# Optimization experiments

Hardware: AMD Instinct MI355X
Metric: run time of the kernel (lower is better)

The kernel has to match this reference:

```python
import jax, jax.numpy as jnp
import numpy as np

B, H, W, C = 1, 180, 360, 192
WS, SHIFT, NH = 6, 3, 6
MLAT, MLON = H // WS, W // WS
NW = MLAT * MLON
N = WS * WS
HD = C // NH
SCALE = HD ** -0.5
EPS = 1e-5


def _rel_index():
    # earth-specific relative position index: (MLAT, N, N) int32
    ch = np.arange(WS)
    cw = np.arange(WS)
    coords = np.stack(np.meshgrid(ch, cw, indexing='ij')).reshape(2, -1)  # (2, N)
    rel = coords[:, :, None] - coords[:, None, :]                         # (2, N, N)
    idx = (rel[0] + WS - 1) * (2 * WS - 1) + (rel[1] + WS - 1)            # (N, N)
    off = np.arange(MLAT) * (2 * WS - 1) * (2 * WS - 1)                   # per-latitude offset
    return (idx[None, :, :] + off[:, None, None]).astype(np.int32)


def _attn_mask():
    # standard shifted-window mask: (NW, N, N), 0 or -100
    img = np.zeros((H, W), dtype=np.int32)
    cnt = 0
    for hs in (slice(0, -WS), slice(-WS, -SHIFT), slice(-SHIFT, None)):
        for ws_ in (slice(0, -WS), slice(-WS, -SHIFT), slice(-SHIFT, None)):
            img[hs, ws_] = cnt
            cnt += 1
    wins = img.reshape(MLAT, WS, MLON, WS).transpose(0, 2, 1, 3).reshape(NW, N)
    diff = wins[:, None, :] - wins[:, :, None]
    return np.where(diff != 0, -100.0, 0.0).astype(np.float32)

_RPI = jnp.asarray(_rel_index())     # (MLAT, N, N)
_MASK = jnp.asarray(_attn_mask())    # (NW, N, N)


def _layernorm(x, g, b):
    mu = jnp.mean(x, axis=-1, keepdims=True)
    var = jnp.mean(jnp.square(x - mu), axis=-1, keepdims=True)
    return (x - mu) * jax.lax.rsqrt(var + EPS) * g + b


def _window_partition(x):
    # (B, H, W, C) -> (B*NW, N, C)
    x = x.reshape(B, MLAT, WS, MLON, WS, C).transpose(0, 1, 3, 2, 4, 5)
    return x.reshape(B * NW, N, C)


def _window_reverse(w):
    # (B*NW, N, C) -> (B, H, W, C)
    x = w.reshape(B, MLAT, MLON, WS, WS, C).transpose(0, 1, 3, 2, 4, 5)
    return x.reshape(B, H, W, C)


def setup_inputs() -> dict:
    key = jax.random.key(0)
    ks = jax.random.split(key, 6)
    s = 0.02
    return {
        'x': jax.random.normal(ks[0], (B, H * W, C), jnp.float32),
        'norm1_w': jnp.ones((C,), jnp.float32),
        'norm1_b': jnp.zeros((C,), jnp.float32),
        'qkv_w': jax.random.normal(ks[1], (C, 3 * C), jnp.float32) * s,
        'qkv_b': jnp.zeros((3 * C,), jnp.float32),
        'proj_w': jax.random.normal(ks[2], (C, C), jnp.float32) * s,
        'proj_b': jnp.zeros((C,), jnp.float32),
        'bias_table': jax.random.normal(ks[3], (MLAT * (2 * WS - 1) ** 2, NH), jnp.float32) * s,
        'norm2_w': jnp.ones((C,), jnp.float32),
        'norm2_b': jnp.zeros((C,), jnp.float32),
        'fc1_w': jax.random.normal(ks[4], (C, 4 * C), jnp.float32) * s,
        'fc1_b': jnp.zeros((4 * C,), jnp.float32),
        'fc2_w': jax.random.normal(ks[5], (4 * C, C), jnp.float32) * s,
        'fc2_b': jnp.zeros((C,), jnp.float32),
    }


def reference(x, norm1_w, norm1_b, qkv_w, qkv_b, proj_w, proj_b, bias_table,
              norm2_w, norm2_b, fc1_w, fc1_b, fc2_w, fc2_b):
    shortcut = x
    h = _layernorm(x, norm1_w, norm1_b).reshape(B, H, W, C)
    # cyclic shift
    h = jnp.roll(h, shift=(-SHIFT, -SHIFT), axis=(1, 2))
    xw = _window_partition(h)                                   # (B*NW, N, C)

    qkv = xw @ qkv_w + qkv_b                                    # (B_, N, 3C)
    qkv = qkv.reshape(B * NW, N, 3, NH, HD).transpose(2, 0, 3, 1, 4)
    q, k, v = qkv[0], qkv[1], qkv[2]                            # (B_, NH, N, HD)

    # earth-specific relative position bias, gathered per latitude row
    bias = jnp.take(bias_table, _RPI, axis=0)                   # (MLAT, N, N, NH)
    bias = bias.transpose(0, 3, 1, 2)[:, None]                  # (MLAT, 1, NH, N, N)
    bias = jnp.broadcast_to(bias, (MLAT, MLON, NH, N, N)).reshape(NW, NH, N, N)
    bias = bias + _MASK[:, None]                                # add shift mask

    attn = jnp.einsum('bhnd,bhmd->bhnm', q, k) * SCALE + bias
    attn = jax.nn.softmax(attn, axis=-1)
    av = jnp.einsum('bhnm,bhmd->bhnd', attn, v)                 # (B_, NH, N, HD)
    av = av.transpose(0, 2, 1, 3).reshape(B * NW, N, C)
    av = av @ proj_w + proj_b

    h = _window_reverse(av)
    h = jnp.roll(h, shift=(SHIFT, SHIFT), axis=(1, 2)).reshape(B, H * W, C)
    x = shortcut + h

    m = _layernorm(x, norm2_w, norm2_b)
    m = jax.nn.gelu(m @ fc1_w + fc1_b, approximate=False) @ fc2_w + fc2_b
    return x + m
```

## Files before the change

### kernel.cpp

```cpp
#include <hip/hip_runtime.h>
#include <hip/hip_bf16.h>

constexpr int HH   = 180;
constexpr int WW   = 360;
constexpr int CC   = 192;
constexpr int WS   = 6;
constexpr int SHIFT= 3;
constexpr int NH   = 6;
constexpr int MLAT = HH / WS;
constexpr int MLON = WW / WS;
constexpr int NWIN = MLAT * MLON;
constexpr int NTOK = WS * WS;
constexpr int HD   = CC / NH;
constexpr long M_TOK = (long)NWIN * NTOK;
constexpr long M_PAD = 65024;
constexpr float SCALE_F = 0.17677669529663687f;

typedef unsigned short ushort_t;
using bf16x8 = __attribute__((ext_vector_type(8))) short;
using f32x4  = __attribute__((ext_vector_type(4))) float;

static __device__ inline float b2f(ushort_t u) {
    union { float f; unsigned int i; } v; v.i = ((unsigned int)u) << 16; return v.f;
}
static __device__ inline ushort_t f2b(float f) {
    __hip_bfloat16 h = __float2bfloat16(f);
    return *(ushort_t*)&h;
}
static __device__ inline unsigned int cvtpk(float lo, float hi) {
    unsigned int r;
    asm("v_cvt_pk_bf16_f32 %0, %1, %2" : "=v"(r) : "v"(lo), "v"(hi));
    return r;
}

static __device__ inline void gload_lds16(const ushort_t* g, ushort_t* l) {
    __builtin_amdgcn_global_load_lds(
        (const __attribute__((address_space(1))) unsigned int*)g,
        (__attribute__((address_space(3))) unsigned int*)l, 16, 0, 0);
}

__global__ void transpose_f2b(const float* __restrict__ in, ushort_t* __restrict__ out,
                              int K, int N) {
    int e = blockIdx.x * 256 + threadIdx.x;
    if (e >= K * N) return;
    int n = e / K, k = e - n * K;
    out[e] = f2b(in[(long)k * N + n]);
}

__global__ void zero_bf16(ushort_t* __restrict__ p, int count) {
    int e = blockIdx.x * 256 + threadIdx.x;
    if (e < count) p[e] = 0;
}

static __device__ inline int region1d(int p, int L) {
    return (p < L - WS) ? 0 : ((p < L - SHIFT) ? 1 : 2);
}

__global__ void bias_mask_precompute(const float* __restrict__ bt, float* __restrict__ bm) {
    int idx = blockIdx.x * 256 + threadIdx.x;
    if (idx >= MLAT * 2 * NH * 36 * 48) return;
    int e = idx;
    int j = e % 48; e /= 48;
    int i = e % 36; e /= 36;
    int h = e % NH; e /= NH;
    int lt = e % 2;
    int mlat = e / 2;
    if (j >= 36) { bm[idx] = -1e30f; return; }
    int ih = i / WS, iw = i - ih * WS;
    int jh = j / WS, jw = j - jh * WS;
    int bidx = mlat * 121 + (ih - jh + 5) * 11 + (iw - jw + 5);
    float v = bt[bidx * NH + h];
    int mlon = lt ? (MLON - 1) : 0;
    int ri = region1d(mlat * WS + ih, HH) * 3 + region1d(mlon * WS + iw, WW);
    int rj = region1d(mlat * WS + jh, HH) * 3 + region1d(mlon * WS + jw, WW);
    if (ri != rj) v += -100.0f;
    bm[idx] = v;
}

__global__ __launch_bounds__(256) void ln1_window_kernel(
    const float* __restrict__ x, const float* __restrict__ g, const float* __restrict__ b,
    ushort_t* __restrict__ xw)
{
    long t = (long)blockIdx.x * 4 + (threadIdx.x >> 6);
    int lane = threadIdx.x & 63;
    if (t >= M_PAD) return;
    if (t >= M_TOK) {
        ushort_t* o = xw + t * CC;
        o[lane] = 0; o[lane + 64] = 0; o[lane + 128] = 0;
        return;
    }
    int ti = (int)t;
    int w = ti / NTOK, n = ti - w * NTOK;
    int mlat = w / MLON, mlon = w - mlat * MLON;
    int sh = mlat * WS + n / WS, sw = mlon * WS + (n % WS);
    int hh = sh + SHIFT; if (hh >= HH) hh -= HH;
    int ww = sw + SHIFT; if (ww >= WW) ww -= WW;
    const float* row = x + ((long)hh * WW + ww) * CC;
    float v0 = row[lane], v1 = row[lane + 64], v2 = row[lane + 128];
    float s = v0 + v1 + v2;
    float ss = v0 * v0 + v1 * v1 + v2 * v2;
    #pragma unroll
    for (int o = 32; o > 0; o >>= 1) { s += __shfl_xor(s, o, 64); ss += __shfl_xor(ss, o, 64); }
    float mu = s * (1.0f / CC);
    float var = ss * (1.0f / CC) - mu * mu;
    float rinv = rsqrtf(var + 1e-5f);
    ushort_t* o = xw + t * CC;
    o[lane]       = f2b((v0 - mu) * rinv * g[lane]       + b[lane]);
    o[lane + 64]  = f2b((v1 - mu) * rinv * g[lane + 64]  + b[lane + 64]);
    o[lane + 128] = f2b((v2 - mu) * rinv * g[lane + 128] + b[lane + 128]);
}

__global__ __launch_bounds__(256) void ln2_kernel(
    const float* __restrict__ xin, const float* __restrict__ g, const float* __restrict__ b,
    ushort_t* __restrict__ h2)
{
    long t = (long)blockIdx.x * 4 + (threadIdx.x >> 6);
    int lane = threadIdx.x & 63;
    if (t >= M_PAD) return;
    if (t >= M_TOK) {
        ushort_t* o = h2 + t * CC;
        o[lane] = 0; o[lane + 64] = 0; o[lane + 128] = 0;
        return;
    }
    const float* row = xin + t * CC;
    float v0 = row[lane], v1 = row[lane + 64], v2 = row[lane + 128];
    float s = v0 + v1 + v2;
    float ss = v0 * v0 + v1 * v1 + v2 * v2;
    #pragma unroll
    for (int o = 32; o > 0; o >>= 1) { s += __shfl_xor(s, o, 64); ss += __shfl_xor(ss, o, 64); }
    float mu = s * (1.0f / CC);
    float var = ss * (1.0f / CC) - mu * mu;
    float rinv = rsqrtf(var + 1e-5f);
    ushort_t* o = h2 + t * CC;
    o[lane]       = f2b((v0 - mu) * rinv * g[lane]       + b[lane]);
    o[lane + 64]  = f2b((v1 - mu) * rinv * g[lane + 64]  + b[lane + 64]);
    o[lane + 128] = f2b((v2 - mu) * rinv * g[lane + 128] + b[lane + 128]);
}

#define BM 128
#define BN 192
#define BK 32

template<int MODE, int KK>
__global__ __launch_bounds__(512, 3) void gemm_bf16(
    const ushort_t* __restrict__ A, const ushort_t* __restrict__ Bt,
    const float* __restrict__ bias,
    ushort_t* __restrict__ outb, float* __restrict__ outf,
    const float* __restrict__ resid,
    int N, long Mguard, int ncol, int nwg)
{
    constexpr int nk = KK / BK;
    __shared__ __align__(16) ushort_t lds[20480];
    __shared__ int row_map[BM];

    int tid = threadIdx.x;
    int lane = tid & 63;
    int wid = tid >> 6;
    int lr = lane & 15, lg = lane >> 4;
    int wm = wid >> 2, wn = wid & 3;

    int orig = blockIdx.x;
    int q = nwg >> 3, r8 = nwg & 7;
    int xcd = orig & 7, pos = orig >> 3;
    int wg = (xcd < r8 ? xcd * (q + 1) : r8 * (q + 1) + (xcd - r8) * q) + pos;
    int brow = wg / ncol, bcol = wg - brow * ncol;
    long bm0 = (long)brow * BM;
    int n0 = bcol * BN;

    if (MODE == 2 && tid < BM) {
        long t = bm0 + tid;
        if (t < M_TOK) {
            int ti = (int)t;
            int w = ti / NTOK, n = ti - w * NTOK;
            int mlat = w / MLON, mlon = w - mlat * MLON;
            int sh = mlat * WS + n / WS, sw = mlon * WS + (n % WS);
            int hh = sh + SHIFT; if (hh >= HH) hh -= HH;
            int wv = sw + SHIFT; if (wv >= WW) wv -= WW;
            row_map[tid] = hh * WW + wv;
        } else row_map[tid] = -1;
    }

    int a_pos  = tid * 16;
    int a_row  = a_pos >> 6, a_cb = a_pos & 63;
    int a_scol = (a_cb ^ ((a_row & 3) << 4)) >> 1;
    int b_row  = a_row, b_scol = a_scol;
    int b2_pos = 8192 + a_pos;
    int b2_row = b2_pos >> 6, b2_cb = b2_pos & 63;
    int b2_scol = (b2_cb ^ ((b2_row & 3) << 4)) >> 1;

#define STAGE(b, k0) do { \
    char* base = (char*)lds + (b) * 20480; \
    gload_lds16(&A[(bm0 + a_row) * KK + (k0) + a_scol], (ushort_t*)(base + a_pos)); \
    gload_lds16(&Bt[(long)(n0 + b_row) * KK + (k0) + b_scol], (ushort_t*)(base + 8192 + a_pos)); \
    if (tid < 256) \
        gload_lds16(&Bt[(long)(n0 + b2_row) * KK + (k0) + b2_scol], (ushort_t*)(base + 8192 + b2_pos)); \
} while (0)

    f32x4 acc[4][3] = {};

    STAGE(0, 0);
    __syncthreads();

    int xr = (lr & 3) << 4;

    #pragma unroll
    for (int kt = 0; kt < nk; ++kt) {
        if (kt + 1 < nk) STAGE((kt + 1) & 1, (kt + 1) * BK);
        const char* base = (const char*)lds + (kt & 1) * 20480;
        bf16x8 af[4], bfr[3];
        #pragma unroll
        for (int fm = 0; fm < 4; ++fm) {
            int row = wm * 64 + fm * 16 + lr;
            af[fm] = *(const bf16x8*)(base + row * 64 + ((lg * 16) ^ xr));
        }
        #pragma unroll
        for (int fn = 0; fn < 3; ++fn) {
            int row = wn * 48 + fn * 16 + lr;
            bfr[fn] = *(const bf16x8*)(base + 8192 + row * 64 + ((lg * 16) ^ xr));
        }
        #pragma unroll
        for (int fm = 0; fm < 4; ++fm)
            #pragma unroll
            for (int fn = 0; fn < 3; ++fn)
                acc[fm][fn] = __builtin_amdgcn_mfma_f32_16x16x32_bf16(af[fm], bfr[fn], acc[fm][fn], 0, 0, 0);
        __syncthreads();
    }
#undef STAGE

    float bv[3];
    #pragma unroll
    for (int fn = 0; fn < 3; ++fn) bv[fn] = bias[n0 + wn * 48 + fn * 16 + lr];

    if (MODE == 0 || MODE == 1) {
        ushort_t* bb = lds + wid * 768;
        #pragma unroll
        for (int fm = 0; fm < 4; ++fm) {
            #pragma unroll
            for (int fn = 0; fn < 3; ++fn) {
                #pragma unroll
                for (int r = 0; r < 4; ++r) {
                    float v = acc[fm][fn][r] + bv[fn];
                    if (MODE == 0) {
                        if (n0 == 0) v *= SCALE_F;
                    }
                    if (MODE == 1) {
                        float e2 = exp2f(v * -2.4556617f);
                        v = v * __builtin_amdgcn_rcpf(1.0f + e2);
                    }
                    bb[(lg * 4 + r) * 48 + fn * 16 + lr] = f2b(v);
                }
            }
            #pragma unroll
            for (int i = 0; i < 2; ++i) {
                int cid = i * 64 + lane;
                if (cid < 96) {
                    int row = cid / 6, c6 = cid - row * 6;
                    uint4 val = *(const uint4*)&bb[row * 48 + c6 * 8];
                    long grow = bm0 + wm * 64 + fm * 16 + row;
                    *(uint4*)&outb[grow * (long)N + n0 + wn * 48 + c6 * 8] = val;
                }
            }
        }
    } else {
        float* fb = (float*)lds + wid * 768;
        #pragma unroll
        for (int fm = 0; fm < 4; ++fm) {
            #pragma unroll
            for (int fn = 0; fn < 3; ++fn)
                #pragma unroll
                for (int r = 0; r < 4; ++r)
                    fb[(lg * 4 + r) * 48 + fn * 16 + lr] = acc[fm][fn][r] + bv[fn];
            #pragma unroll
            for (int i = 0; i < 3; ++i) {
                int cid = i * 64 + lane;
                int row = cid / 12, c4 = cid - row * 12;
                f32x4 val = *(const f32x4*)&fb[row * 48 + c4 * 4];
                int lrow = wm * 64 + fm * 16 + row;
                int col = wn * 48 + c4 * 4;
                if (MODE == 3) {
                    long grow = bm0 + lrow;
                    if (grow < Mguard) {
                        float* p = &outf[grow * 192 + col];
                        f32x4 old = *(const f32x4*)p;
                        *(f32x4*)p = old + val;
                    }
                } else {
                    int pp = row_map[lrow];
                    if (pp >= 0) {
                        const float* rp = &resid[(long)pp * 192 + col];
                        f32x4 rv = *(const f32x4*)rp;
                        *(f32x4*)&outf[(long)pp * 192 + col] = rv + val;
                    }
                }
            }
        }
    }
}

__global__ __launch_bounds__(256) void attn_mfma_kernel(
    const ushort_t* __restrict__ qkv,
    const float* __restrict__ bm,
    ushort_t* __restrict__ av)
{
    int wid = threadIdx.x >> 6, lane = threadIdx.x & 63;
    int unit = blockIdx.x * 4 + wid;
    int w = unit / NH, h = unit - (unit / NH) * NH;
    int mlat = w / MLON, mlon = w - mlat * MLON;
    int lr = lane & 15, lg = lane >> 4;

    const ushort_t* Qb = qkv + (long)w * NTOK * 576 + h * HD;
    const ushort_t* Kb = Qb + 192;
    const ushort_t* Vb = Qb + 384;

    bf16x8 kf[3], qf[3];
    #pragma unroll
    for (int t = 0; t < 3; ++t) {
        kf[t] = *(const bf16x8*)&Kb[(long)(t * 16 + lr) * 576 + 8 * lg];
        qf[t] = *(const bf16x8*)&Qb[(long)(t * 16 + lr) * 576 + 8 * lg];
    }
    f32x4 st[3][3] = {};
    #pragma unroll
    for (int mt = 0; mt < 3; ++mt)
        #pragma unroll
        for (int qt = 0; qt < 3; ++qt)
            st[mt][qt] = __builtin_amdgcn_mfma_f32_16x16x32_bf16(kf[mt], qf[qt], st[mt][qt], 0, 0, 0);

    bf16x8 vf[2][2];
    #pragma unroll
    for (int nd = 0; nd < 2; ++nd)
        #pragma unroll
        for (int kt = 0; kt < 2; ++kt)
            #pragma unroll
            for (int j = 0; j < 8; ++j)
                ((short*)&vf[nd][kt])[j] =
                    (short)Vb[(long)(kt * 32 + 8 * lg + j) * 576 + nd * 16 + lr];

    const float* bb = bm + (((mlat * 2 + (mlon == MLON - 1)) * NH) + h) * (36 * 48);

    f32x4 o[2][3] = {};
    int src0 = ((2 * (lg & 1)) << 4) | lr;
    int src1 = src0 + 16;

    #pragma unroll
    for (int qt = 0; qt < 3; ++qt) {
        int qrow = qt * 16 + lr;
        int qq = qrow < 36 ? qrow : 35;
        float v[3][4];
        #pragma unroll
        for (int mt = 0; mt < 3; ++mt) {
            f32x4 b4 = *(const f32x4*)&bb[qq * 48 + mt * 16 + 4 * lg];
            #pragma unroll
            for (int r = 0; r < 4; ++r) v[mt][r] = st[mt][qt][r] + b4[r];
        }
        float mx = v[0][0];
        #pragma unroll
        for (int mt = 0; mt < 3; ++mt)
            #pragma unroll
            for (int r = 0; r < 4; ++r) mx = fmaxf(mx, v[mt][r]);
        mx = fmaxf(mx, __shfl_xor(mx, 16, 64));
        mx = fmaxf(mx, __shfl_xor(mx, 32, 64));
        float p[3][4], sum = 0.f;
        #pragma unroll
        for (int mt = 0; mt < 3; ++mt)
            #pragma unroll
            for (int r = 0; r < 4; ++r) { p[mt][r] = __expf(v[mt][r] - mx); sum += p[mt][r]; }
        sum += __shfl_xor(sum, 16, 64);
        sum += __shfl_xor(sum, 32, 64);
        float rs = 1.0f / sum;

        unsigned int pk[3][2];
        #pragma unroll
        for (int mt = 0; mt < 3; ++mt) {
            pk[mt][0] = cvtpk(p[mt][0] * rs, p[mt][1] * rs);
            pk[mt][1] = cvtpk(p[mt][2] * rs, p[mt][3] * rs);
        }
        unsigned int f0[4], f1[4];
        {
            unsigned int a, b;
            a = (unsigned)__shfl((int)pk[0][0], src0, 64); b = (unsigned)__shfl((int)pk[1][0], src0, 64);
            f0[0] = (lg < 2) ? a : b;
            a = (unsigned)__shfl((int)pk[0][1], src0, 64); b = (unsigned)__shfl((int)pk[1][1], src0, 64);
            f0[1] = (lg < 2) ? a : b;
            a = (unsigned)__shfl((int)pk[0][0], src1, 64); b = (unsigned)__shfl((int)pk[1][0], src1, 64);
            f0[2] = (lg < 2) ? a : b;
            a = (unsigned)__shfl((int)pk[0][1], src1, 64); b = (unsigned)__shfl((int)pk[1][1], src1, 64);
            f0[3] = (lg < 2) ? a : b;
            f1[0] = (lg < 2) ? (unsigned)__shfl((int)pk[2][0], src0, 64) : 0u;
            f1[1] = (lg < 2) ? (unsigned)__shfl((int)pk[2][1], src0, 64) : 0u;
            f1[2] = (lg < 2) ? (unsigned)__shfl((int)pk[2][0], src1, 64) : 0u;
            f1[3] = (lg < 2) ? (unsigned)__shfl((int)pk[2][1], src1, 64) : 0u;
        }
        union { unsigned int u[4]; bf16x8 v8; } pf0, pf1;
        pf0.u[0] = f0[0]; pf0.u[1] = f0[1]; pf0.u[2] = f0[2]; pf0.u[3] = f0[3];
        pf1.u[0] = f1[0]; pf1.u[1] = f1[1]; pf1.u[2] = f1[2]; pf1.u[3] = f1[3];

        #pragma unroll
        for (int nd = 0; nd < 2; ++nd) {
            o[nd][qt] = __builtin_amdgcn_mfma_f32_16x16x32_bf16(vf[nd][0], pf0.v8, o[nd][qt], 0, 0, 0);
            o[nd][qt] = __builtin_amdgcn_mfma_f32_16x16x32_bf16(vf[nd][1], pf1.v8, o[nd][qt], 0, 0, 0);
        }
    }

    #pragma unroll
    for (int qt = 0; qt < 3; ++qt) {
        int qrow = qt * 16 + lr;
        if (qrow < NTOK) {
            #pragma unroll
            for (int nd = 0; nd < 2; ++nd) {
                uint2 pkd;
                pkd.x = cvtpk(o[nd][qt][0], o[nd][qt][1]);
                pkd.y = cvtpk(o[nd][qt][2], o[nd][qt][3]);
                *(uint2*)&av[((long)w * NTOK + qrow) * CC + h * HD + nd * 16 + 4 * lg] = pkd;
            }
        }
    }
}

extern "C" void kernel_launch(void* const* d_in, const int* in_sizes, int n_in,
                              void* d_out, int out_size, void* d_ws, size_t ws_size,
                              hipStream_t stream) {
    const float* x        = (const float*)d_in[0];
    const float* n1w      = (const float*)d_in[1];
    const float* n1b      = (const float*)d_in[2];
    const float* qkv_w    = (const float*)d_in[3];
    const float* qkv_b    = (const float*)d_in[4];
    const float* proj_w   = (const float*)d_in[5];
    const float* proj_b   = (const float*)d_in[6];
    const float* btab     = (const float*)d_in[7];
    const float* n2w      = (const float*)d_in[8];
    const float* n2b      = (const float*)d_in[9];
    const float* fc1_w    = (const float*)d_in[10];
    const float* fc1_b    = (const float*)d_in[11];
    const float* fc2_w    = (const float*)d_in[12];
    const float* fc2_b    = (const float*)d_in[13];
    float* out = (float*)d_out;

    char* p = (char*)d_ws;
    ushort_t* xw  = (ushort_t*)p;  p += M_PAD * 192 * 2;
    ushort_t* big = (ushort_t*)p;  p += M_PAD * 768 * 2;
    ushort_t* av  = (ushort_t*)p;  p += M_PAD * 192 * 2;
    ushort_t* wqkv = (ushort_t*)p; p += 576 * 192 * 2;
    ushort_t* wproj= (ushort_t*)p; p += 192 * 192 * 2;
    ushort_t* wfc1 = (ushort_t*)p; p += 768 * 192 * 2;
    ushort_t* wfc2 = (ushort_t*)p; p += 192 * 768 * 2;
    float*    bmask= (float*)p;    p += MLAT * 2 * NH * 36 * 48 * 4;

    transpose_f2b<<<(576*192 + 255)/256, 256, 0, stream>>>(qkv_w, wqkv, 192, 576);
    transpose_f2b<<<(192*192 + 255)/256, 256, 0, stream>>>(proj_w, wproj, 192, 192);
    transpose_f2b<<<(768*192 + 255)/256, 256, 0, stream>>>(fc1_w, wfc1, 192, 768);
    transpose_f2b<<<(192*768 + 255)/256, 256, 0, stream>>>(fc2_w, wfc2, 768, 192);
    bias_mask_precompute<<<(MLAT*2*NH*36*48 + 255)/256, 256, 0, stream>>>(btab, bmask);
    zero_bf16<<<((int)(M_PAD - M_TOK)*192 + 255)/256, 256, 0, stream>>>(av + M_TOK * 192, (int)(M_PAD - M_TOK) * 192);

    ln1_window_kernel<<<M_PAD / 4, 256, 0, stream>>>(x, n1w, n1b, xw);

    gemm_bf16<0, 192><<<508 * 3, 512, 0, stream>>>(
        xw, wqkv, qkv_b, big, nullptr, nullptr, 576, M_PAD, 3, 508 * 3);

    attn_mfma_kernel<<<NWIN * NH / 4, 256, 0, stream>>>(big, bmask, av);

    gemm_bf16<2, 192><<<508, 512, 0, stream>>>(
        av, wproj, proj_b, nullptr, out, x, 192, M_TOK, 1, 508);

    ln2_kernel<<<M_PAD / 4, 256, 0, stream>>>(out, n2w, n2b, xw);

    gemm_bf16<1, 192><<<508 * 4, 512, 0, stream>>>(
        xw, wfc1, fc1_b, big, nullptr, nullptr, 768, M_PAD, 4, 508 * 4);

    gemm_bf16<3, 768><<<508, 512, 0, stream>>>(
        big, wfc2, fc2_b, nullptr, out, nullptr, 192, M_TOK, 1, 508);
}
```

Baseline: 201.8 us.

## Restructure GEMM to 64-row tiles with whole-K A staging and register-held B

The bf16 GEMM now uses 64-row tiles with 4 waves, each wave owning 48 output columns. Each 192-wide K chunk of A is staged into LDS in one pass with an 8-row XOR swizzle, and B fragments are read straight from global memory into registers, prefetched two k-steps ahead. The aim is fewer barriers and less LDS traffic per MFMA, plus double the workgroup count for better occupancy and load balance. In exchange, B reads are no longer shared across waves through LDS, so global/L2 traffic for weights goes up, and the fc2 path loses double buffering across its four K chunks.

```diff
diff --git a/kernel.cpp b/kernel.cpp
--- a/kernel.cpp
+++ b/kernel.cpp
@@ -137,27 +137,25 @@
     o[lane + 128] = f2b((v2 - mu) * rinv * g[lane + 128] + b[lane + 128]);
 }
 
-#define BM 128
+#define BM 64
 #define BN 192
-#define BK 32
 
 template<int MODE, int KK>
-__global__ __launch_bounds__(512, 3) void gemm_bf16(
+__global__ __launch_bounds__(256, 3) void gemm_bf16(
     const ushort_t* __restrict__ A, const ushort_t* __restrict__ Bt,
     const float* __restrict__ bias,
     ushort_t* __restrict__ outb, float* __restrict__ outf,
     const float* __restrict__ resid,
     int N, long Mguard, int ncol, int nwg)
 {
-    constexpr int nk = KK / BK;
-    __shared__ __align__(16) ushort_t lds[20480];
+    constexpr int NCH = KK / 192;
+    __shared__ __align__(16) ushort_t lds[64 * 192];
     __shared__ int row_map[BM];
 
     int tid = threadIdx.x;
     int lane = tid & 63;
-    int wid = tid >> 6;
+    int wn = tid >> 6;
     int lr = lane & 15, lg = lane >> 4;
-    int wm = wid >> 2, wn = wid & 3;
 
     int orig = blockIdx.x;
     int q = nwg >> 3, r8 = nwg & 7;
@@ -180,59 +178,73 @@
         } else row_map[tid] = -1;
     }
 
-    int a_pos  = tid * 16;
-    int a_row  = a_pos >> 6, a_cb = a_pos & 63;
-    int a_scol = (a_cb ^ ((a_row & 3) << 4)) >> 1;
-    int b_row  = a_row, b_scol = a_scol;
-    int b2_pos = 8192 + a_pos;
-    int b2_row = b2_pos >> 6, b2_cb = b2_pos & 63;
-    int b2_scol = (b2_cb ^ ((b2_row & 3) << 4)) >> 1;
-
-#define STAGE(b, k0) do { \
-    char* base = (char*)lds + (b) * 20480; \
-    gload_lds16(&A[(bm0 + a_row) * KK + (k0) + a_scol], (ushort_t*)(base + a_pos)); \
-    gload_lds16(&Bt[(long)(n0 + b_row) * KK + (k0) + b_scol], (ushort_t*)(base + 8192 + a_pos)); \
-    if (tid < 256) \
-        gload_lds16(&Bt[(long)(n0 + b2_row) * KK + (k0) + b2_scol], (ushort_t*)(base + 8192 + b2_pos)); \
-} while (0)
+    int s_a   = tid * 16;
+    int s_row[6], s_col[6];
+    #pragma unroll
+    for (int i = 0; i < 6; ++i) {
+        int a = s_a + i * 4096;
+        int row = a / 384, b = a - row * 384;
+        s_row[i] = row;
+        s_col[i] = (b ^ ((row & 7) << 4)) >> 1;
+    }
+
+    const ushort_t* Bw = Bt + (long)(n0 + wn * 48) * KK;
+    int xr = (lr & 7) << 4;
 
     f32x4 acc[4][3] = {};
 
-    STAGE(0, 0);
-    __syncthreads();
-
-    int xr = (lr & 3) << 4;
-
-    #pragma unroll
-    for (int kt = 0; kt < nk; ++kt) {
-        if (kt + 1 < nk) STAGE((kt + 1) & 1, (kt + 1) * BK);
-        const char* base = (const char*)lds + (kt & 1) * 20480;
-        bf16x8 af[4], bfr[3];
-        #pragma unroll
-        for (int fm = 0; fm < 4; ++fm) {
-            int row = wm * 64 + fm * 16 + lr;
-            af[fm] = *(const bf16x8*)(base + row * 64 + ((lg * 16) ^ xr));
-        }
-        #pragma unroll
-        for (int fn = 0; fn < 3; ++fn) {
-            int row = wn * 48 + fn * 16 + lr;
-            bfr[fn] = *(const bf16x8*)(base + 8192 + row * 64 + ((lg * 16) ^ xr));
-        }
-        #pragma unroll
-        for (int fm = 0; fm < 4; ++fm)
+    #pragma unroll
+    for (int ch = 0; ch < NCH; ++ch) {
+        int k0 = ch * 192;
+        if (ch > 0) {
+            asm volatile("s_waitcnt lgkmcnt(0)" ::: "memory");
+            __builtin_amdgcn_s_barrier();
+        }
+        #pragma unroll
+        for (int i = 0; i < 6; ++i)
+            gload_lds16(&A[(bm0 + s_row[i]) * KK + k0 + s_col[i]],
+                        &lds[(s_a + i * 4096) >> 1]);
+
+        bf16x8 bfr[6][3];
+        #pragma unroll
+        for (int kt = 0; kt < 2; ++kt)
             #pragma unroll
             for (int fn = 0; fn < 3; ++fn)
-                acc[fm][fn] = __builtin_amdgcn_mfma_f32_16x16x32_bf16(af[fm], bfr[fn], acc[fm][fn], 0, 0, 0);
-        __syncthreads();
-    }
-#undef STAGE
+                bfr[kt][fn] = *(const bf16x8*)&Bw[(long)(fn * 16 + lr) * KK + k0 + kt * 32 + 8 * lg];
+
+        asm volatile("s_waitcnt vmcnt(0)" ::: "memory");
+        __builtin_amdgcn_s_barrier();
+
+        #pragma unroll
+        for (int kt = 0; kt < 6; ++kt) {
+            if (kt < 4) {
+                #pragma unroll
+                for (int fn = 0; fn < 3; ++fn)
+                    bfr[kt + 2][fn] = *(const bf16x8*)&Bw[(long)(fn * 16 + lr) * KK + k0 + (kt + 2) * 32 + 8 * lg];
+            }
+            bf16x8 af[4];
+            #pragma unroll
+            for (int fm = 0; fm < 4; ++fm)
+                af[fm] = *(const bf16x8*)((const char*)lds + (fm * 16 + lr) * 384 + ((kt * 64 + lg * 16) ^ xr));
+            __builtin_amdgcn_s_setprio(1);
+            #pragma unroll
+            for (int fm = 0; fm < 4; ++fm)
+                #pragma unroll
+                for (int fn = 0; fn < 3; ++fn)
+                    acc[fm][fn] = __builtin_amdgcn_mfma_f32_16x16x32_bf16(af[fm], bfr[kt][fn], acc[fm][fn], 0, 0, 0);
+            __builtin_amdgcn_s_setprio(0);
+        }
+    }
+
+    asm volatile("s_waitcnt lgkmcnt(0)" ::: "memory");
+    __builtin_amdgcn_s_barrier();
 
     float bv[3];
     #pragma unroll
     for (int fn = 0; fn < 3; ++fn) bv[fn] = bias[n0 + wn * 48 + fn * 16 + lr];
 
     if (MODE == 0 || MODE == 1) {
-        ushort_t* bb = lds + wid * 768;
+        ushort_t* bb = lds + wn * 768;
         #pragma unroll
         for (int fm = 0; fm < 4; ++fm) {
             #pragma unroll
@@ -256,13 +268,13 @@
                 if (cid < 96) {
                     int row = cid / 6, c6 = cid - row * 6;
                     uint4 val = *(const uint4*)&bb[row * 48 + c6 * 8];
-                    long grow = bm0 + wm * 64 + fm * 16 + row;
+                    long grow = bm0 + fm * 16 + row;
                     *(uint4*)&outb[grow * (long)N + n0 + wn * 48 + c6 * 8] = val;
                 }
             }
         }
     } else {
-        float* fb = (float*)lds + wid * 768;
+        float* fb = (float*)lds + wn * 768;
         #pragma unroll
         for (int fm = 0; fm < 4; ++fm) {
             #pragma unroll
@@ -275,7 +287,7 @@
                 int cid = i * 64 + lane;
                 int row = cid / 12, c4 = cid - row * 12;
                 f32x4 val = *(const f32x4*)&fb[row * 48 + c4 * 4];
-                int lrow = wm * 64 + fm * 16 + row;
+                int lrow = fm * 16 + row;
                 int col = wn * 48 + c4 * 4;
                 if (MODE == 3) {
                     long grow = bm0 + lrow;
@@ -454,19 +466,19 @@
 
     ln1_window_kernel<<<M_PAD / 4, 256, 0, stream>>>(x, n1w, n1b, xw);
 
-    gemm_bf16<0, 192><<<508 * 3, 512, 0, stream>>>(
-        xw, wqkv, qkv_b, big, nullptr, nullptr, 576, M_PAD, 3, 508 * 3);
+    gemm_bf16<0, 192><<<1016 * 3, 256, 0, stream>>>(
+        xw, wqkv, qkv_b, big, nullptr, nullptr, 576, M_PAD, 3, 1016 * 3);
 
     attn_mfma_kernel<<<NWIN * NH / 4, 256, 0, stream>>>(big, bmask, av);
 
-    gemm_bf16<2, 192><<<508, 512, 0, stream>>>(
-        av, wproj, proj_b, nullptr, out, x, 192, M_TOK, 1, 508);
+    gemm_bf16<2, 192><<<1016, 256, 0, stream>>>(
+        av, wproj, proj_b, nullptr, out, x, 192, M_TOK, 1, 1016);
 
     ln2_kernel<<<M_PAD / 4, 256, 0, stream>>>(out, n2w, n2b, xw);
 
-    gemm_bf16<1, 192><<<508 * 4, 512, 0, stream>>>(
-        xw, wfc1, fc1_b, big, nullptr, nullptr, 768, M_PAD, 4, 508 * 4);
-
-    gemm_bf16<3, 768><<<508, 512, 0, stream>>>(
-        big, wfc2, fc2_b, nullptr, out, nullptr, 192, M_TOK, 1, 508);
-}
+    gemm_bf16<1, 192><<<1016 * 4, 256, 0, stream>>>(
+        xw, wfc1, fc1_b, big, nullptr, nullptr, 768, M_PAD, 4, 1016 * 4);
+
+    gemm_bf16<3, 768><<<1016, 256, 0, stream>>>(
+        big, wfc2, fc2_b, nullptr, out, nullptr, 192, M_TOK, 1, 1016);
+}
```

New measurement: 233.0 us. +15.5%, slower.

## Merge weight transposes into one launch and tune GEMM K-loop synchronization

Applied to the files above, without the earlier changes.

The four weight transpose-and-convert launches become a single kernel that picks its source and destination matrix from the element index, which removes launch overhead. In the GEMM K-loop, each __syncthreads is replaced by explicit vmcnt waits sized to each wave's in-flight loads, plain s_barrier calls, and an lgkmcnt wait. The MFMA block is wrapped in raised s_setprio. The aim is to let the next tile's global-to-LDS loads overlap compute with tighter waits. This depends on the vmcnt counts matching each wave's issued loads, or stale LDS data could be read.

```diff
diff --git a/kernel.cpp b/kernel.cpp
--- a/kernel.cpp
+++ b/kernel.cpp
@@ -39,10 +39,17 @@
         (__attribute__((address_space(3))) unsigned int*)l, 16, 0, 0);
 }
 
-__global__ void transpose_f2b(const float* __restrict__ in, ushort_t* __restrict__ out,
-                              int K, int N) {
+__global__ void transpose_all(const float* __restrict__ qkv_w, const float* __restrict__ proj_w,
+                              const float* __restrict__ fc1_w, const float* __restrict__ fc2_w,
+                              ushort_t* __restrict__ wqkv, ushort_t* __restrict__ wproj,
+                              ushort_t* __restrict__ wfc1, ushort_t* __restrict__ wfc2) {
     int e = blockIdx.x * 256 + threadIdx.x;
-    if (e >= K * N) return;
+    const float* in; ushort_t* out; int K, N;
+    if (e < 110592)      { in = qkv_w;  out = wqkv;  K = 192; N = 576; }
+    else if (e < 147456) { e -= 110592; in = proj_w; out = wproj; K = 192; N = 192; }
+    else if (e < 294912) { e -= 147456; in = fc1_w;  out = wfc1;  K = 192; N = 768; }
+    else if (e < 442368) { e -= 294912; in = fc2_w;  out = wfc2;  K = 768; N = 192; }
+    else return;
     int n = e / K, k = e - n * K;
     out[e] = f2b(in[(long)k * N + n]);
 }
@@ -199,13 +206,22 @@
     f32x4 acc[4][3] = {};
 
     STAGE(0, 0);
-    __syncthreads();
+    asm volatile("s_waitcnt vmcnt(0)" ::: "memory");
+    __builtin_amdgcn_s_barrier();
 
     int xr = (lr & 3) << 4;
 
     #pragma unroll
     for (int kt = 0; kt < nk; ++kt) {
-        if (kt + 1 < nk) STAGE((kt + 1) & 1, (kt + 1) * BK);
+        if (kt + 1 < nk) {
+            STAGE((kt + 1) & 1, (kt + 1) * BK);
+            if (wid < 4) asm volatile("s_waitcnt vmcnt(3)" ::: "memory");
+            else         asm volatile("s_waitcnt vmcnt(2)" ::: "memory");
+        } else {
+            asm volatile("s_waitcnt vmcnt(0)" ::: "memory");
+        }
+        __builtin_amdgcn_s_barrier();
+
         const char* base = (const char*)lds + (kt & 1) * 20480;
         bf16x8 af[4], bfr[3];
         #pragma unroll
@@ -218,12 +234,15 @@
             int row = wn * 48 + fn * 16 + lr;
             bfr[fn] = *(const bf16x8*)(base + 8192 + row * 64 + ((lg * 16) ^ xr));
         }
+        __builtin_amdgcn_s_setprio(1);
         #pragma unroll
         for (int fm = 0; fm < 4; ++fm)
             #pragma unroll
             for (int fn = 0; fn < 3; ++fn)
                 acc[fm][fn] = __builtin_amdgcn_mfma_f32_16x16x32_bf16(af[fm], bfr[fn], acc[fm][fn], 0, 0, 0);
-        __syncthreads();
+        __builtin_amdgcn_s_setprio(0);
+        asm volatile("s_waitcnt lgkmcnt(0)" ::: "memory");
+        __builtin_amdgcn_s_barrier();
     }
 #undef STAGE
 
@@ -256,7 +275,7 @@
                 if (cid < 96) {
                     int row = cid / 6, c6 = cid - row * 6;
                     uint4 val = *(const uint4*)&bb[row * 48 + c6 * 8];
-                    long grow = bm0 + wm * 64 + fm * 16 + row;
+                    long grow = bm0 + fm * 16 + row + wm * 64;
                     *(uint4*)&outb[grow * (long)N + n0 + wn * 48 + c6 * 8] = val;
                 }
             }
@@ -445,10 +464,8 @@
     ushort_t* wfc2 = (ushort_t*)p; p += 192 * 768 * 2;
     float*    bmask= (float*)p;    p += MLAT * 2 * NH * 36 * 48 * 4;
 
-    transpose_f2b<<<(576*192 + 255)/256, 256, 0, stream>>>(qkv_w, wqkv, 192, 576);
-    transpose_f2b<<<(192*192 + 255)/256, 256, 0, stream>>>(proj_w, wproj, 192, 192);
-    transpose_f2b<<<(768*192 + 255)/256, 256, 0, stream>>>(fc1_w, wfc1, 192, 768);
-    transpose_f2b<<<(192*768 + 255)/256, 256, 0, stream>>>(fc2_w, wfc2, 768, 192);
+    transpose_all<<<(442368 + 255)/256, 256, 0, stream>>>(
+        qkv_w, proj_w, fc1_w, fc2_w, wqkv, wproj, wfc1, wfc2);
     bias_mask_precompute<<<(MLAT*2*NH*36*48 + 255)/256, 256, 0, stream>>>(btab, bmask);
     zero_bf16<<<((int)(M_PAD - M_TOK)*192 + 255)/256, 256, 0, stream>>>(av + M_TOK * 192, (int)(M_PAD - M_TOK) * 192);
 
```

Result: faster. 195.5 us (-3.1%).
